# Kernel tuning notes

Hardware: AMD Instinct MI355X
Metric: run time of the kernel (lower is better)

## Reference

```python
import jax, jax.numpy as jnp
import numpy as np

Q = 64  # truncation_q


def _gelu(x):
    return jax.nn.gelu(x, approximate=False)  # torch nn.GELU default (erf)


def setup_inputs() -> dict:
    key = jax.random.key(0)
    ks = jax.random.split(key, 12)
    n, d = 256, 4096            # x_shape_0, x_shape_1
    hid, y0, y1 = 4096, 512, 4096
    cin = d + d                 # x_shape_1 + cov_dim
    s = lambda f: 1.0 / np.sqrt(f)
    return {
        "X": jax.random.normal(ks[0], (n, d), jnp.float32),
        # weight_net: Linear(1,64)->GELU->Linear(64,1)
        "wn_w1": jax.random.normal(ks[1], (1, 64), jnp.float32),
        "wn_b1": jnp.zeros((64,), jnp.float32),
        "wn_w2": jax.random.normal(ks[2], (64, 1), jnp.float32) * s(64),
        "wn_b2": jnp.zeros((1,), jnp.float32),
        # MLP
        "fc1_w": jax.random.normal(ks[3], (hid, cin), jnp.float32) * s(cin),
        "fc1_b": jnp.zeros((hid,), jnp.float32),
        "fc2_w": jax.random.normal(ks[4], (hid, hid), jnp.float32) * s(hid),
        "fc2_b": jnp.zeros((hid,), jnp.float32),
        "fc3_w": jax.random.normal(ks[5], (y1, hid), jnp.float32) * s(hid),
        "fc3_b": jnp.zeros((y1,), jnp.float32),
        "proj": jax.random.normal(ks[6], (y0, n), jnp.float32),
    }


def _lr_cov(X, wn_w1, wn_b1, wn_w2, wn_b2):
    # X: [n, d]. Vectorized replacement of the python double loop:
    # gamma_l[i,j] = (1/d) sum_t (X[i,t]-m_i)(X[j,t+l]-m_j), l=0..Q; gamma_{-l} = gamma_l^T
    n, d = X.shape
    Xc = X - jnp.mean(X, axis=1, keepdims=True)

    def gamma(ell):
        mask = (jnp.arange(d) < d - ell).astype(X.dtype)      # zero out wrapped tail
        Y = jnp.roll(Xc, -ell, axis=1) * mask                  # [n, d]
        return (Xc @ Y.T) / d                                  # [n, n]

    G_pos = jax.vmap(gamma)(jnp.arange(Q + 1))                 # [Q+1, n, n], l = 0..Q
    G_neg = jnp.flip(jnp.transpose(G_pos[1:], (0, 2, 1)), axis=0)  # l = -Q..-1
    G = jnp.concatenate([G_neg, G_pos], axis=0)                # [2Q+1, n, n]

    lags = jnp.arange(-Q, Q + 1, dtype=X.dtype)[:, None]       # [2Q+1, 1]
    h = _gelu(lags @ wn_w1 + wn_b1)
    w = (h @ wn_w2 + wn_b2)[:, 0]                              # [2Q+1]
    return jnp.einsum("l,lij->ij", w, G)                       # weighted long-run cov


def reference(X, wn_w1, wn_b1, wn_w2, wn_b2, fc1_w, fc1_b, fc2_w, fc2_b, fc3_w, fc3_b, proj):
    cov = _lr_cov(X, wn_w1, wn_b1, wn_w2, wn_b2)               # [n, n]
    cov_inter = cov @ X                                        # [n, d]
    z = jnp.concatenate([X, cov_inter], axis=1)                # [n, 2d]
    out = _gelu(z @ fc1_w.T + fc1_b)
    out = _gelu(out @ fc2_w.T + fc2_b)
    out = out @ fc3_w.T + fc3_b                                # [n, y1]
    return proj @ out                                          # [y0, y1]
```

## Files before the change

kernel.cpp:

```cpp
#include <hip/hip_runtime.h>
#include <math.h>

typedef float  f32x4 __attribute__((ext_vector_type(4)));
typedef _Float16 f16x8 __attribute__((ext_vector_type(8)));
typedef _Float16 f16x4 __attribute__((ext_vector_type(4)));

__device__ __forceinline__ float gelu_f(float x) {
    return 0.5f * x * (1.0f + erff(x * 0.70710678118654752440f));
}

__device__ __forceinline__ f16x4 cvt4(float4 v) {
    f16x4 h;
    h.x = (_Float16)v.x; h.y = (_Float16)v.y;
    h.z = (_Float16)v.z; h.w = (_Float16)v.w;
    return h;
}

__global__ void weightnet_kernel(const float* __restrict__ w1, const float* __restrict__ b1,
                                 const float* __restrict__ w2, const float* __restrict__ b2,
                                 float* __restrict__ wout) {
    int l = threadIdx.x;
    if (l < 129) {
        float lag = (float)(l - 64);
        float acc = b2[0];
        for (int k = 0; k < 64; ++k) {
            float h = lag * w1[k] + b1[k];
            acc += gelu_f(h) * w2[k];
        }
        wout[l] = acc;
    }
}

__global__ __launch_bounds__(256)
void center_conv_kernel(const float* __restrict__ X,
                        const float* __restrict__ w, float* __restrict__ Xc,
                        float* __restrict__ Y, float* __restrict__ z) {
    __shared__ float xs[4224];
    __shared__ float wsm[132];
    __shared__ float ps[4];
    const int j = blockIdx.x, tid = threadIdx.x;
    float4* xs4 = (float4*)xs;

    if (tid < 64) { xs[tid] = 0.f; xs[4160 + tid] = 0.f; }
    if (tid < 132) wsm[tid] = (tid < 129) ? w[tid] : 0.f;

    const float4* Xr4 = (const float4*)(X + (size_t)j * 4096);
    float4* zr4 = (float4*)(z + (size_t)j * 8192);
    float s = 0.f;
    float4 vbuf[4];
    #pragma unroll
    for (int k = 0; k < 4; ++k) {
        int c4 = tid + k * 256;
        float4 v = Xr4[c4];
        vbuf[k] = v;
        xs4[16 + c4] = v;
        zr4[c4] = v;
        s += v.x + v.y + v.z + v.w;
    }
    #pragma unroll
    for (int o = 32; o > 0; o >>= 1) s += __shfl_down(s, o, 64);
    if ((tid & 63) == 0) ps[tid >> 6] = s;
    __syncthreads();
    const float m = (ps[0] + ps[1] + ps[2] + ps[3]) * (1.0f / 4096.0f);

    float4* Xc4 = (float4*)(Xc + (size_t)j * 4096);
    #pragma unroll
    for (int k = 0; k < 4; ++k) {
        int c4 = tid + k * 256;
        float4 v = vbuf[k];
        v.x -= m; v.y -= m; v.z -= m; v.w -= m;
        xs4[16 + c4] = v;
        Xc4[c4] = v;
    }
    __syncthreads();

    float4 acc[4] = {};
    float4 xv[4];
    #pragma unroll
    for (int b = 0; b < 4; ++b) xv[b] = xs4[tid + b * 256];
    #pragma unroll
    for (int jg = 0; jg < 32; ++jg) {
        float4 wv = *(const float4*)&wsm[4 * jg];
        #pragma unroll
        for (int b = 0; b < 4; ++b) {
            float4 xn = xs4[tid + b * 256 + jg + 1];
            acc[b].x += wv.x * xv[b].x + wv.y * xv[b].y + wv.z * xv[b].z + wv.w * xv[b].w;
            acc[b].y += wv.x * xv[b].y + wv.y * xv[b].z + wv.z * xv[b].w + wv.w * xn.x;
            acc[b].z += wv.x * xv[b].z + wv.y * xv[b].w + wv.z * xn.x  + wv.w * xn.y;
            acc[b].w += wv.x * xv[b].w + wv.y * xn.x  + wv.z * xn.y  + wv.w * xn.z;
            xv[b] = xn;
        }
    }
    const float w128 = wsm[128];
    float4* Yr4 = (float4*)(Y + (size_t)j * 4096);
    #pragma unroll
    for (int b = 0; b < 4; ++b) {
        acc[b].x += w128 * xv[b].x; acc[b].y += w128 * xv[b].y;
        acc[b].z += w128 * xv[b].z; acc[b].w += w128 * xv[b].w;
        Yr4[tid + b * 256] = acc[b];
    }
}

__global__ void transpose_kernel(const float* __restrict__ in, float* __restrict__ out,
                                 int R, int C) {
    __shared__ float t[32][33];
    int bx = blockIdx.x * 32;
    int by = blockIdx.y * 32;
    int tx = threadIdx.x & 31, ty = threadIdx.x >> 5;
    #pragma unroll
    for (int i = ty; i < 32; i += 8)
        t[i][tx] = in[(size_t)(by + i) * C + bx + tx];
    __syncthreads();
    #pragma unroll
    for (int i = ty; i < 32; i += 8)
        out[(size_t)(bx + i) * R + by + tx] = t[tx][i];
}

template<int GELU>
__global__ void reduce_kernel(const float* __restrict__ P, size_t zstride, int S,
                              const float* __restrict__ bias, float scale,
                              float* __restrict__ out, int ncols4, int outstride4) {
    int idx = blockIdx.x * 256 + threadIdx.x;
    float4 a = ((const float4*)P)[idx];
    for (int s = 1; s < S; ++s) {
        float4 p = ((const float4*)(P + (size_t)s * zstride))[idx];
        a.x += p.x; a.y += p.y; a.z += p.z; a.w += p.w;
    }
    a.x *= scale; a.y *= scale; a.z *= scale; a.w *= scale;
    int row = idx / ncols4, col4 = idx - row * ncols4;
    if (bias) {
        float4 b = ((const float4*)bias)[col4];
        a.x += b.x; a.y += b.y; a.z += b.z; a.w += b.w;
    }
    if (GELU) {
        a.x = gelu_f(a.x); a.y = gelu_f(a.y);
        a.z = gelu_f(a.z); a.w = gelu_f(a.w);
    }
    ((float4*)out)[(size_t)row * outstride4 + col4] = a;
}

#define LDS_GRP 136
__global__ __launch_bounds__(256, 2)
void gemm_bt(const float* __restrict__ A, int lda,
             const float* __restrict__ B, int ldb,
             float* __restrict__ P, int ldc, size_t zstride,
             int K_chunk) {
    __shared__ _Float16 sA[64 * LDS_GRP];
    __shared__ _Float16 sB[64 * LDS_GRP];
    const int tid  = threadIdx.x;
    const int wv   = tid >> 6, lane = tid & 63;
    const int wm   = (wv >> 1) * 64, wn = (wv & 1) * 64;
    const int quad = lane >> 4, l16 = lane & 15;
    const int srow = tid >> 4;
    const int sk   = (tid & 15) * 4;

    const size_t k0 = (size_t)blockIdx.z * (size_t)K_chunk;
    const float* Ab = A + (size_t)blockIdx.x * 128 * (size_t)lda + k0;
    const float* Bb = B + (size_t)blockIdx.y * 128 * (size_t)ldb + k0;

    const int wroff = (sk >> 3) * LDS_GRP + srow * 8 + (sk & 4);

    f32x4 acc[4][4] = {};
    float4 av[8], bv[8];
    #pragma unroll
    for (int p = 0; p < 8; ++p) {
        av[p] = *(const float4*)(Ab + (size_t)(p * 16 + srow) * lda + sk);
        bv[p] = *(const float4*)(Bb + (size_t)(p * 16 + srow) * ldb + sk);
    }

    const int nk = K_chunk >> 6;
    for (int kt = 0; ; ++kt) {
        __syncthreads();
        #pragma unroll
        for (int p = 0; p < 8; ++p) {
            int off = p * 8 * LDS_GRP + wroff;
            *(f16x4*)&sA[off] = cvt4(av[p]);
            *(f16x4*)&sB[off] = cvt4(bv[p]);
        }
        __syncthreads();
        if (kt + 1 < nk) {
            const float* An = Ab + (size_t)(kt + 1) * 64;
            const float* Bn = Bb + (size_t)(kt + 1) * 64;
            #pragma unroll
            for (int p = 0; p < 8; ++p) {
                av[p] = *(const float4*)(An + (size_t)(p * 16 + srow) * lda + sk);
                bv[p] = *(const float4*)(Bn + (size_t)(p * 16 + srow) * ldb + sk);
            }
        }
        #pragma unroll
        for (int ks = 0; ks < 2; ++ks) {
            f16x8 af[4], bfr[4];
            #pragma unroll
            for (int i = 0; i < 4; ++i) {
                af[i]  = *(const f16x8*)&sA[(((wm >> 4) + i) * 8 + ks * 4 + quad) * LDS_GRP + l16 * 8];
                bfr[i] = *(const f16x8*)&sB[(((wn >> 4) + i) * 8 + ks * 4 + quad) * LDS_GRP + l16 * 8];
            }
            #pragma unroll
            for (int mi = 0; mi < 4; ++mi)
                #pragma unroll
                for (int ni = 0; ni < 4; ++ni)
                    acc[mi][ni] = __builtin_amdgcn_mfma_f32_16x16x32_f16(af[mi], bfr[ni], acc[mi][ni], 0, 0, 0);
        }
        if (kt + 1 >= nk) break;
    }

    float* Cp = P + (size_t)blockIdx.z * zstride;
    #pragma unroll
    for (int mi = 0; mi < 4; ++mi)
        #pragma unroll
        for (int ni = 0; ni < 4; ++ni) {
            size_t colg = (size_t)blockIdx.y * 128 + wn + ni * 16 + l16;
            #pragma unroll
            for (int rr = 0; rr < 4; ++rr) {
                size_t rowg = (size_t)blockIdx.x * 128 + wm + mi * 16 + quad * 4 + rr;
                Cp[rowg * (size_t)ldc + colg] = acc[mi][ni][rr];
            }
        }
}

extern "C" void kernel_launch(void* const* d_in, const int* in_sizes, int n_in,
                              void* d_out, int out_size, void* d_ws, size_t ws_size,
                              hipStream_t stream) {
    const float* X    = (const float*)d_in[0];
    const float* wnw1 = (const float*)d_in[1];
    const float* wnb1 = (const float*)d_in[2];
    const float* wnw2 = (const float*)d_in[3];
    const float* wnb2 = (const float*)d_in[4];
    const float* fc1w = (const float*)d_in[5];
    const float* fc1b = (const float*)d_in[6];
    const float* fc2w = (const float*)d_in[7];
    const float* fc2b = (const float*)d_in[8];
    const float* fc3w = (const float*)d_in[9];
    const float* fc3b = (const float*)d_in[10];
    const float* proj = (const float*)d_in[11];
    float* out = (float*)d_out;

    float* ws   = (float*)d_ws;
    float* z    = ws;
    float* h1   = z   + 2097152;
    float* h2   = h1  + 1048576;
    float* cov  = h2  + 1048576;
    float* wbuf = cov + 65536;
    float* P    = wbuf + 256;
    float* Xc   = P;
    float* Yb   = P + 1048576;
    float* XT   = P + 2097152;
    float* Pcov = P + 3145728;
    float* h3   = h1;
    float* h3T  = h2;

    weightnet_kernel<<<1, 192, 0, stream>>>(wnw1, wnb1, wnw2, wnb2, wbuf);
    center_conv_kernel<<<256, 256, 0, stream>>>(X, wbuf, Xc, Yb, z);
    transpose_kernel<<<dim3(128, 8), 256, 0, stream>>>(X, XT, 256, 4096);

    gemm_bt<<<dim3(2, 2, 32), 256, 0, stream>>>(Xc, 4096, Yb, 4096, Pcov, 256, 65536, 128);
    reduce_kernel<0><<<64, 256, 0, stream>>>(Pcov, 65536, 32, nullptr, 1.0f / 4096.0f, cov, 64, 64);

    gemm_bt<<<dim3(2, 32, 2), 256, 0, stream>>>(cov, 256, XT, 256, P, 4096, 1048576, 128);
    reduce_kernel<0><<<1024, 256, 0, stream>>>(P, 1048576, 2, nullptr, 1.0f, z + 4096, 1024, 2048);

    gemm_bt<<<dim3(2, 32, 8), 256, 0, stream>>>(z, 8192, fc1w, 8192, P, 4096, 1048576, 1024);
    reduce_kernel<1><<<1024, 256, 0, stream>>>(P, 1048576, 8, fc1b, 1.0f, h1, 1024, 1024);

    gemm_bt<<<dim3(2, 32, 8), 256, 0, stream>>>(h1, 4096, fc2w, 4096, P, 4096, 1048576, 512);
    reduce_kernel<1><<<1024, 256, 0, stream>>>(P, 1048576, 8, fc2b, 1.0f, h2, 1024, 1024);

    gemm_bt<<<dim3(2, 32, 8), 256, 0, stream>>>(h2, 4096, fc3w, 4096, P, 4096, 1048576, 512);
    reduce_kernel<0><<<1024, 256, 0, stream>>>(P, 1048576, 8, fc3b, 1.0f, h3, 1024, 1024);

    transpose_kernel<<<dim3(128, 8), 256, 0, stream>>>(h3, h3T, 256, 4096);

    gemm_bt<<<dim3(4, 32, 2), 256, 0, stream>>>(proj, 256, h3T, 256, P, 4096, 2097152, 128);
    reduce_kernel<0><<<2048, 256, 0, stream>>>(P, 2097152, 2, nullptr, 1.0f, out, 1024, 1024);
}
```

Measured before the change: 465.5 us.

## Double-buffer LDS tiles with K=32 steps and two-deep register prefetch in GEMM

The GEMM main loop is restructured to use two LDS buffers of half the K depth (32 instead of 64) and two sets of prefetch registers, loading global tiles two steps ahead. This drops one of the two barriers per iteration and overlaps the LDS store of the next tile with MFMA on the current one. In exchange there are twice as many iterations, and the extra register sets and smaller K steps may raise register pressure or per-iteration overhead.

```diff
diff --git a/kernel.cpp b/kernel.cpp
--- a/kernel.cpp
+++ b/kernel.cpp
@@ -145,64 +145,80 @@
              const float* __restrict__ B, int ldb,
              float* __restrict__ P, int ldc, size_t zstride,
              int K_chunk) {
-    __shared__ _Float16 sA[64 * LDS_GRP];
-    __shared__ _Float16 sB[64 * LDS_GRP];
+    __shared__ _Float16 sA[2][32 * LDS_GRP];
+    __shared__ _Float16 sB[2][32 * LDS_GRP];
     const int tid  = threadIdx.x;
     const int wv   = tid >> 6, lane = tid & 63;
     const int wm   = (wv >> 1) * 64, wn = (wv & 1) * 64;
     const int quad = lane >> 4, l16 = lane & 15;
-    const int srow = tid >> 4;
-    const int sk   = (tid & 15) * 4;
+    const int srow = tid >> 3;
+    const int sk   = (tid & 7) * 4;
+    const int koct = sk >> 3;
+    const int k4   = sk & 4;
 
     const size_t k0 = (size_t)blockIdx.z * (size_t)K_chunk;
     const float* Ab = A + (size_t)blockIdx.x * 128 * (size_t)lda + k0;
     const float* Bb = B + (size_t)blockIdx.y * 128 * (size_t)ldb + k0;
 
-    const int wroff = (sk >> 3) * LDS_GRP + srow * 8 + (sk & 4);
-
     f32x4 acc[4][4] = {};
-    float4 av[8], bv[8];
-    #pragma unroll
-    for (int p = 0; p < 8; ++p) {
-        av[p] = *(const float4*)(Ab + (size_t)(p * 16 + srow) * lda + sk);
-        bv[p] = *(const float4*)(Bb + (size_t)(p * 16 + srow) * ldb + sk);
-    }
-
-    const int nk = K_chunk >> 6;
-    for (int kt = 0; ; ++kt) {
+    float4 a0[4], b0[4], a1[4], b1[4];
+
+#define LOADT(aset, bset, kt_) do {                                          \
+    const float* An_ = Ab + (size_t)(kt_) * 32;                              \
+    const float* Bn_ = Bb + (size_t)(kt_) * 32;                              \
+    _Pragma("unroll")                                                        \
+    for (int p = 0; p < 4; ++p) {                                            \
+        aset[p] = *(const float4*)(An_ + (size_t)(p * 32 + srow) * lda + sk);\
+        bset[p] = *(const float4*)(Bn_ + (size_t)(p * 32 + srow) * ldb + sk);\
+    } } while (0)
+
+#define STORET(buf_, aset, bset) do {                                        \
+    _Pragma("unroll")                                                        \
+    for (int p = 0; p < 4; ++p) {                                            \
+        int off = ((p * 2 + (srow >> 4)) * 4 + koct) * LDS_GRP               \
+                  + (srow & 15) * 8 + k4;                                    \
+        *(f16x4*)&sA[buf_][off] = cvt4(aset[p]);                             \
+        *(f16x4*)&sB[buf_][off] = cvt4(bset[p]);                             \
+    } } while (0)
+
+#define MFMAT(buf_) do {                                                     \
+    f16x8 af[4], bfr[4];                                                     \
+    _Pragma("unroll")                                                        \
+    for (int i = 0; i < 4; ++i) {                                            \
+        af[i]  = *(const f16x8*)&sA[buf_][(((wm >> 4) + i) * 4 + quad) * LDS_GRP + l16 * 8]; \
+        bfr[i] = *(const f16x8*)&sB[buf_][(((wn >> 4) + i) * 4 + quad) * LDS_GRP + l16 * 8]; \
+    }                                                                        \
+    _Pragma("unroll")                                                        \
+    for (int mi = 0; mi < 4; ++mi)                                           \
+        _Pragma("unroll")                                                    \
+        for (int ni = 0; ni < 4; ++ni)                                       \
+            acc[mi][ni] = __builtin_amdgcn_mfma_f32_16x16x32_f16(af[mi], bfr[ni], acc[mi][ni], 0, 0, 0); \
+    } while (0)
+
+    const int nk = K_chunk >> 5;
+    LOADT(a0, b0, 0);
+    if (nk > 1) LOADT(a1, b1, 1);
+    STORET(0, a0, b0);
+    if (nk > 2) LOADT(a0, b0, 2);
+    __syncthreads();
+
+    for (int kt = 0; kt < nk; ++kt) {
+        const int cur = kt & 1;
+        if (kt + 1 < nk) {
+            if ((kt + 1) & 1) {
+                STORET(cur ^ 1, a1, b1);
+                if (kt + 3 < nk) LOADT(a1, b1, kt + 3);
+            } else {
+                STORET(cur ^ 1, a0, b0);
+                if (kt + 3 < nk) LOADT(a0, b0, kt + 3);
+            }
+        }
+        MFMAT(cur);
         __syncthreads();
-        #pragma unroll
-        for (int p = 0; p < 8; ++p) {
-            int off = p * 8 * LDS_GRP + wroff;
-            *(f16x4*)&sA[off] = cvt4(av[p]);
-            *(f16x4*)&sB[off] = cvt4(bv[p]);
-        }
-        __syncthreads();
-        if (kt + 1 < nk) {
-            const float* An = Ab + (size_t)(kt + 1) * 64;
-            const float* Bn = Bb + (size_t)(kt + 1) * 64;
-            #pragma unroll
-            for (int p = 0; p < 8; ++p) {
-                av[p] = *(const float4*)(An + (size_t)(p * 16 + srow) * lda + sk);
-                bv[p] = *(const float4*)(Bn + (size_t)(p * 16 + srow) * ldb + sk);
-            }
-        }
-        #pragma unroll
-        for (int ks = 0; ks < 2; ++ks) {
-            f16x8 af[4], bfr[4];
-            #pragma unroll
-            for (int i = 0; i < 4; ++i) {
-                af[i]  = *(const f16x8*)&sA[(((wm >> 4) + i) * 8 + ks * 4 + quad) * LDS_GRP + l16 * 8];
-                bfr[i] = *(const f16x8*)&sB[(((wn >> 4) + i) * 8 + ks * 4 + quad) * LDS_GRP + l16 * 8];
-            }
-            #pragma unroll
-            for (int mi = 0; mi < 4; ++mi)
-                #pragma unroll
-                for (int ni = 0; ni < 4; ++ni)
-                    acc[mi][ni] = __builtin_amdgcn_mfma_f32_16x16x32_f16(af[mi], bfr[ni], acc[mi][ni], 0, 0, 0);
-        }
-        if (kt + 1 >= nk) break;
-    }
+    }
+#undef LOADT
+#undef STORET
+#undef MFMAT
 
     float* Cp = P + (size_t)blockIdx.z * zstride;
     #pragma unroll
```

Result: faster. 454.5 us (-2.4%).
